# Kernel tuning notes

Measured on AMD Instinct MI355X. Metric: run time of the kernel, lower is better.

The kernel has to match this reference:

```python
import jax, jax.numpy as jnp
import numpy as np

B, T, E, H = 2, 2048, 1024, 16
D = E // H  # head_dim = 64


def setup_inputs() -> dict:
    key = jax.random.key(0)
    ks = jax.random.split(key, 7)
    s = 1.0 / np.sqrt(E)
    queries = jax.random.normal(ks[0], (B, T, E), dtype=jnp.float32)
    keys = jax.random.normal(ks[1], (B, T, E), dtype=jnp.float32)
    values = jax.random.normal(ks[2], (B, T, E), dtype=jnp.float32)
    # causal mask: True where attention is disallowed (masked_fill semantics)
    mask = jnp.triu(jnp.ones((T, T), dtype=bool), k=1)[None, None]  # [1,1,T,T]
    Wq = jax.random.uniform(ks[3], (E, E), jnp.float32, -s, s)
    Wk = jax.random.uniform(ks[4], (E, E), jnp.float32, -s, s)
    Wv = jax.random.uniform(ks[5], (E, E), jnp.float32, -s, s)
    Wo = jax.random.uniform(ks[6], (E, E), jnp.float32, -s, s)
    return {"queries": queries, "keys": keys, "values": values, "mask": mask,
            "Wq": Wq, "Wk": Wk, "Wv": Wv, "Wo": Wo}


def _split(x):
    # [B,T,E] -> [B,H,T,D]
    return x.reshape(B, T, H, D).transpose(0, 2, 1, 3)


def reference(queries, keys, values, mask, Wq, Wk, Wv, Wo):
    # nn.Linear(E,E,bias=False): y = x @ W.T
    q = _split(queries @ Wq.T)  # [B,H,T,D]
    k = _split(keys @ Wk.T)
    v = _split(values @ Wv.T)
    scores = jnp.einsum('bhqd,bhkd->bhqk', q, k) / jnp.sqrt(jnp.float32(D))
    scores = jnp.where(mask, -jnp.inf, scores)
    weights = jax.nn.softmax(scores, axis=-1)
    attn = jnp.einsum('bhqk,bhkd->bhqd', weights, v)  # [B,H,T,D]
    joined = attn.transpose(0, 2, 1, 3).reshape(B, T, E)
    return joined @ Wo.T
```

## Files before the change

kernel.cpp:

```cpp
#include <hip/hip_runtime.h>
#include <hip/hip_bf16.h>

#define T_DIM 2048
#define E_DIM 1024
#define MM 4096
#define NN 1024
#define KK 1024
#define MSZ ((size_t)MM * KK)
#define WSZ ((size_t)NN * KK)

typedef __attribute__((ext_vector_type(8))) short bh8;
typedef __attribute__((ext_vector_type(4))) short bh4;
typedef __attribute__((ext_vector_type(4))) float fx4;

static __device__ __forceinline__ short f2bf(float f) {
  union { float f; unsigned u; } v; v.f = f;
  unsigned r = (v.u + 0x7fffu + ((v.u >> 16) & 1u)) >> 16;
  return (short)(unsigned short)r;
}

static __device__ __forceinline__ void gload16(const void* g, void* l) {
  __builtin_amdgcn_global_load_lds(
      (const __attribute__((address_space(1))) unsigned*)g,
      (__attribute__((address_space(3))) unsigned*)l, 16, 0, 0);
}

__global__ __launch_bounds__(256) void cvt_w(const float* __restrict__ s0,
                                             const float* __restrict__ s1,
                                             const float* __restrict__ s2,
                                             const float* __restrict__ s3,
                                             short* __restrict__ dst) {
  int a = blockIdx.y;
  const float* sp = a == 0 ? s0 : a == 1 ? s1 : a == 2 ? s2 : s3;
  size_t i = ((size_t)blockIdx.x * 256 + threadIdx.x) * 8;
  fx4 x = *(const fx4*)(sp + i);
  fx4 y = *(const fx4*)(sp + i + 4);
  bh8 o;
#pragma unroll
  for (int j = 0; j < 4; j++) { o[j] = f2bf(x[j]); o[4 + j] = f2bf(y[j]); }
  *(bh8*)(dst + (size_t)a * WSZ + i) = o;
}

__global__ __launch_bounds__(256) void cvt_act(const float* __restrict__ s0,
                                               const float* __restrict__ s1,
                                               const float* __restrict__ s2,
                                               short* __restrict__ dst) {
  int a = blockIdx.y;
  const float* sp = a == 0 ? s0 : a == 1 ? s1 : s2;
  size_t i = ((size_t)blockIdx.x * 256 + threadIdx.x) * 8;
  fx4 x = *(const fx4*)(sp + i);
  fx4 y = *(const fx4*)(sp + i + 4);
  bh8 o;
#pragma unroll
  for (int j = 0; j < 4; j++) { o[j] = f2bf(x[j]); o[4 + j] = f2bf(y[j]); }
  *(bh8*)(dst + (size_t)a * MSZ + i) = o;
}

template<bool AF32, bool OUTF32>
__global__ __launch_bounds__(256) void gemm_fast(const void* __restrict__ A0,
                                                 const void* __restrict__ A1,
                                                 const void* __restrict__ A2,
                                                 const short* __restrict__ W0,
                                                 void* __restrict__ C0)
{
  __shared__ short As[128 * 32];
  __shared__ short Bs[128 * 32];
  const int tid = threadIdx.x;
  const int lane = tid & 63, w = tid >> 6;
  const int lm = lane & 15, lg = lane >> 4;
  const int wr = w >> 1, wc = w & 1;
  const int m0 = blockIdx.y * 128, n0 = blockIdx.x * 128;
  const int z = blockIdx.z;
  const void* Ap = z == 0 ? A0 : z == 1 ? A1 : A2;
  const short* W = W0 + (size_t)z * WSZ;

  fx4 acc[4][4] = {};

  for (int k0 = 0; k0 < KK; k0 += 32) {
    __syncthreads();
#pragma unroll
    for (int c = 0; c < 2; c++) {
      int idx = c * 256 + tid;
      int row = idx >> 2, kc = idx & 3;
      gload16(W + (size_t)(n0 + row) * KK + k0 + kc * 8, Bs + idx * 8);
      if constexpr (AF32) {
        const float* Af = (const float*)Ap;
        const float* src = Af + (size_t)(m0 + row) * KK + k0 + kc * 8;
        fx4 x = *(const fx4*)src;
        fx4 y = *(const fx4*)(src + 4);
        bh8 o;
#pragma unroll
        for (int j = 0; j < 4; j++) { o[j] = f2bf(x[j]); o[4 + j] = f2bf(y[j]); }
        *(bh8*)&As[idx * 8] = o;
      } else {
        const short* Ab = (const short*)Ap;
        gload16(Ab + (size_t)(m0 + row) * KK + k0 + kc * 8, As + idx * 8);
      }
    }
    __syncthreads();
    bh8 af[4], bf[4];
#pragma unroll
    for (int mi = 0; mi < 4; mi++)
      af[mi] = *(const bh8*)&As[(wr * 64 + mi * 16 + lm) * 32 + lg * 8];
#pragma unroll
    for (int ni = 0; ni < 4; ni++)
      bf[ni] = *(const bh8*)&Bs[(wc * 64 + ni * 16 + lm) * 32 + lg * 8];
#pragma unroll
    for (int mi = 0; mi < 4; mi++)
#pragma unroll
      for (int ni = 0; ni < 4; ni++)
        acc[mi][ni] = __builtin_amdgcn_mfma_f32_16x16x32_bf16(af[mi], bf[ni], acc[mi][ni], 0, 0, 0);
  }

#pragma unroll
  for (int mi = 0; mi < 4; mi++)
#pragma unroll
    for (int ni = 0; ni < 4; ni++) {
      int row = m0 + wr * 64 + mi * 16 + lg * 4;
      int col = n0 + wc * 64 + ni * 16 + lm;
#pragma unroll
      for (int r = 0; r < 4; r++) {
        float vv = acc[mi][ni][r];
        if constexpr (OUTF32) ((float*)C0)[(size_t)z * MSZ + (size_t)(row + r) * NN + col] = vv;
        else ((short*)C0)[(size_t)z * MSZ + (size_t)(row + r) * NN + col] = f2bf(vv);
      }
    }
}

template<bool AF32, bool OUTF32>
__global__ __launch_bounds__(256) void gemm_nt(const void* __restrict__ Ap,
                                               const float* __restrict__ Bw,
                                               void* __restrict__ Cp,
                                               int M, int N, int K)
{
  __shared__ short As[128 * 40];
  __shared__ short Bs[128 * 40];
  const int tid = threadIdx.x;
  const int lane = tid & 63;
  const int w = tid >> 6;
  const int lm = lane & 15;
  const int lg = lane >> 4;
  const int wr = w >> 1, wc = w & 1;
  const int m0 = blockIdx.y * 128, n0 = blockIdx.x * 128;

  fx4 acc[4][4] = {};

  for (int k0 = 0; k0 < K; k0 += 32) {
    __syncthreads();
#pragma unroll
    for (int i = 0; i < 4; ++i) {
      int g = i * 256 + tid;
      int row = g >> 3, cg = g & 7;
      bh4 a4;
      if constexpr (AF32) {
        const float* A = (const float*)Ap;
        fx4 v = *(const fx4*)(A + (size_t)(m0 + row) * K + k0 + cg * 4);
#pragma unroll
        for (int j = 0; j < 4; j++) a4[j] = f2bf(v[j]);
      } else {
        const short* A = (const short*)Ap;
        a4 = *(const bh4*)(A + (size_t)(m0 + row) * K + k0 + cg * 4);
      }
      *(bh4*)&As[row * 40 + cg * 4] = a4;

      fx4 bv = *(const fx4*)(Bw + (size_t)(n0 + row) * K + k0 + cg * 4);
      bh4 b4;
#pragma unroll
      for (int j = 0; j < 4; j++) b4[j] = f2bf(bv[j]);
      *(bh4*)&Bs[row * 40 + cg * 4] = b4;
    }
    __syncthreads();

    bh8 af[4], bf[4];
#pragma unroll
    for (int mi = 0; mi < 4; mi++)
      af[mi] = *(const bh8*)&As[(wr * 64 + mi * 16 + lm) * 40 + lg * 8];
#pragma unroll
    for (int ni = 0; ni < 4; ni++)
      bf[ni] = *(const bh8*)&Bs[(wc * 64 + ni * 16 + lm) * 40 + lg * 8];
#pragma unroll
    for (int mi = 0; mi < 4; mi++)
#pragma unroll
      for (int ni = 0; ni < 4; ni++)
        acc[mi][ni] = __builtin_amdgcn_mfma_f32_16x16x32_bf16(af[mi], bf[ni], acc[mi][ni], 0, 0, 0);
  }

#pragma unroll
  for (int mi = 0; mi < 4; mi++) {
#pragma unroll
    for (int ni = 0; ni < 4; ni++) {
      int row = m0 + wr * 64 + mi * 16 + lg * 4;
      int col = n0 + wc * 64 + ni * 16 + lm;
#pragma unroll
      for (int r = 0; r < 4; r++) {
        float vv = acc[mi][ni][r];
        if constexpr (OUTF32) ((float*)Cp)[(size_t)(row + r) * N + col] = vv;
        else        ((short*)Cp)[(size_t)(row + r) * N + col] = f2bf(vv);
      }
    }
  }
}

__global__ __launch_bounds__(256) void attn_kernel(const short* __restrict__ Q,
                                                   const short* __restrict__ Kb,
                                                   const short* __restrict__ Vb,
                                                   short* __restrict__ At)
{
  __shared__ short Kl[2][64 * 64];
  __shared__ short Vt[2][64 * 64];
  __shared__ short Pl[4 * 16 * 72];

  const int tid = threadIdx.x;
  const int lane = tid & 63;
  const int w = tid >> 6;
  const int lm = lane & 15;
  const int lg = lane >> 4;
  const int pi = blockIdx.x;
  const int bh = blockIdx.y;
  const size_t headoff = (size_t)(bh >> 4) * T_DIM * E_DIM + (size_t)(bh & 15) * 64;

  const int r0 = tid >> 3, ch0 = tid & 7;
  const int r1 = (256 + tid) >> 3, ch1 = tid & 7;

  for (int s = 0; s < 2; s++) {
    const int qt = s ? (31 - pi) : pi;
    const int q0 = qt * 64;

    const int qrow = q0 + w * 16 + lm;
    bh8 qf[2];
#pragma unroll
    for (int ks = 0; ks < 2; ks++)
      qf[ks] = *(const bh8*)(Q + headoff + (size_t)qrow * E_DIM + ks * 32 + lg * 8);

    fx4 oacc[4] = {};
    float m_r[4], l_r[4];
#pragma unroll
    for (int r = 0; r < 4; r++) { m_r[r] = -INFINITY; l_r[r] = 0.0f; }

    {
      gload16(Kb + headoff + (size_t)r0 * E_DIM + ((ch0 ^ (r0 & 7)) * 8), &Kl[0][tid * 8]);
      gload16(Kb + headoff + (size_t)r1 * E_DIM + ((ch1 ^ (r1 & 7)) * 8), &Kl[0][(256 + tid) * 8]);
      bh8 v8a = *(const bh8*)(Vb + headoff + (size_t)r0 * E_DIM + ch0 * 8);
      bh8 v8b = *(const bh8*)(Vb + headoff + (size_t)r1 * E_DIM + ch1 * 8);
#pragma unroll
      for (int j = 0; j < 8; j++) {
        int d = ch0 * 8 + j;
        Vt[0][d * 64 + (((r0 >> 3) ^ ((ch0 + j) & 7)) * 8) + (r0 & 7)] = v8a[j];
        Vt[0][d * 64 + (((r1 >> 3) ^ ((ch1 + j) & 7)) * 8) + (r1 & 7)] = v8b[j];
      }
    }
    __syncthreads();

    int cur = 0;
    for (int t = 0; t <= qt; ++t) {
      const bool pre = (t < qt);
      bh8 v8a, v8b;
      if (pre) {
        const int kvn = (t + 1) * 64;
        gload16(Kb + headoff + (size_t)(kvn + r0) * E_DIM + ((ch0 ^ (r0 & 7)) * 8),
                &Kl[cur ^ 1][tid * 8]);
        gload16(Kb + headoff + (size_t)(kvn + r1) * E_DIM + ((ch1 ^ (r1 & 7)) * 8),
                &Kl[cur ^ 1][(256 + tid) * 8]);
        v8a = *(const bh8*)(Vb + headoff + (size_t)(kvn + r0) * E_DIM + ch0 * 8);
        v8b = *(const bh8*)(Vb + headoff + (size_t)(kvn + r1) * E_DIM + ch1 * 8);
      }

      fx4 sacc[4] = {};
#pragma unroll
      for (int nb = 0; nb < 4; nb++) {
        const int rK = nb * 16 + lm;
#pragma unroll
        for (int ks = 0; ks < 2; ks++) {
          bh8 kf = *(const bh8*)&Kl[cur][rK * 64 + (((ks * 4 + lg) ^ (lm & 7)) * 8)];
          sacc[nb] = __builtin_amdgcn_mfma_f32_16x16x32_bf16(qf[ks], kf, sacc[nb], 0, 0, 0);
        }
      }

      float sv[4][4];
      const bool maskt = (t == qt);
#pragma unroll
      for (int nb = 0; nb < 4; nb++)
#pragma unroll
        for (int r = 0; r < 4; r++) {
          float x = sacc[nb][r] * 0.125f;
          if (maskt && (nb * 16 + lm > w * 16 + lg * 4 + r)) x = -INFINITY;
          sv[nb][r] = x;
        }

      float p[4][4];
#pragma unroll
      for (int r = 0; r < 4; r++) {
        float rm = fmaxf(fmaxf(sv[0][r], sv[1][r]), fmaxf(sv[2][r], sv[3][r]));
#pragma unroll
        for (int off = 1; off < 16; off <<= 1) rm = fmaxf(rm, __shfl_xor(rm, off));
        float mn = fmaxf(m_r[r], rm);
        float fac = __expf(m_r[r] - mn);
        float ps = 0.0f;
#pragma unroll
        for (int nb = 0; nb < 4; nb++) { p[nb][r] = __expf(sv[nb][r] - mn); ps += p[nb][r]; }
#pragma unroll
        for (int off = 1; off < 16; off <<= 1) ps += __shfl_xor(ps, off);
        l_r[r] = l_r[r] * fac + ps;
        m_r[r] = mn;
#pragma unroll
        for (int db = 0; db < 4; db++) oacc[db][r] *= fac;
      }

#pragma unroll
      for (int nb = 0; nb < 4; nb++)
#pragma unroll
        for (int r = 0; r < 4; r++)
          Pl[w * 1152 + (lg * 4 + r) * 72 + nb * 16 + lm] = f2bf(p[nb][r]);

      bh8 pa[2];
#pragma unroll
      for (int ks = 0; ks < 2; ks++)
        pa[ks] = *(const bh8*)&Pl[w * 1152 + lm * 72 + ks * 32 + lg * 8];
#pragma unroll
      for (int db = 0; db < 4; db++) {
        const int d = db * 16 + lm;
        const int gsw = ((d >> 3) + (d & 7)) & 7;
#pragma unroll
        for (int ks = 0; ks < 2; ks++) {
          bh8 vf = *(const bh8*)&Vt[cur][d * 64 + (((ks * 4 + lg) ^ gsw) * 8)];
          oacc[db] = __builtin_amdgcn_mfma_f32_16x16x32_bf16(pa[ks], vf, oacc[db], 0, 0, 0);
        }
      }

      if (pre) {
#pragma unroll
        for (int j = 0; j < 8; j++) {
          int d = ch0 * 8 + j;
          Vt[cur ^ 1][d * 64 + (((r0 >> 3) ^ ((ch0 + j) & 7)) * 8) + (r0 & 7)] = v8a[j];
          Vt[cur ^ 1][d * 64 + (((r1 >> 3) ^ ((ch1 + j) & 7)) * 8) + (r1 & 7)] = v8b[j];
        }
      }
      __syncthreads();
      cur ^= 1;
    }

#pragma unroll
    for (int r = 0; r < 4; r++) {
      float rl = 1.0f / l_r[r];
      int row = q0 + w * 16 + lg * 4 + r;
#pragma unroll
      for (int db = 0; db < 4; db++)
        At[headoff + (size_t)row * E_DIM + db * 16 + lm] = f2bf(oacc[db][r] * rl);
    }
  }
}

extern "C" void kernel_launch(void* const* d_in, const int* in_sizes, int n_in,
                              void* d_out, int out_size, void* d_ws, size_t ws_size,
                              hipStream_t stream)
{
  const float* q  = (const float*)d_in[0];
  const float* k  = (const float*)d_in[1];
  const float* v  = (const float*)d_in[2];
  const float* Wq = (const float*)d_in[4];
  const float* Wk = (const float*)d_in[5];
  const float* Wv = (const float*)d_in[6];
  const float* Wo = (const float*)d_in[7];

  short* Qb  = (short*)d_ws;
  short* Kbb = Qb + MSZ;
  short* Vbb = Kbb + MSZ;
  short* wqb = Vbb + MSZ;
  short* Xq  = wqb + 4 * WSZ;
  short* At  = Xq;

  const size_t need_full = (3 * MSZ + 4 * WSZ + 3 * MSZ) * 2;
  const size_t need_mid  = (4 * MSZ + 4 * WSZ) * 2;

  if (ws_size >= need_full) {
    cvt_act<<<dim3(MSZ / (256 * 8), 3), 256, 0, stream>>>(q, k, v, Xq);
    cvt_w<<<dim3(WSZ / (256 * 8), 4), 256, 0, stream>>>(Wq, Wk, Wv, Wo, wqb);
    gemm_fast<false, false><<<dim3(NN / 128, MM / 128, 3), 256, 0, stream>>>(
        Xq, Xq + MSZ, Xq + 2 * MSZ, wqb, Qb);
    attn_kernel<<<dim3(16, 32), 256, 0, stream>>>(Qb, Kbb, Vbb, At);
    gemm_fast<false, true><<<dim3(NN / 128, MM / 128, 1), 256, 0, stream>>>(
        At, At, At, wqb + 3 * WSZ, d_out);
  } else if (ws_size >= need_mid) {
    short* At2  = Vbb + MSZ;
    short* wqb2 = At2 + MSZ;
    cvt_w<<<dim3(WSZ / (256 * 8), 4), 256, 0, stream>>>(Wq, Wk, Wv, Wo, wqb2);
    gemm_fast<true, false><<<dim3(NN / 128, MM / 128, 3), 256, 0, stream>>>(q, k, v, wqb2, Qb);
    attn_kernel<<<dim3(16, 32), 256, 0, stream>>>(Qb, Kbb, Vbb, At2);
    gemm_fast<false, true><<<dim3(NN / 128, MM / 128, 1), 256, 0, stream>>>(
        At2, At2, At2, wqb2 + 3 * WSZ, d_out);
  } else {
    short* At2 = Vbb + MSZ;
    dim3 gg(NN / 128, MM / 128);
    gemm_nt<true, false><<<gg, 256, 0, stream>>>(q, Wq, Qb, MM, NN, KK);
    gemm_nt<true, false><<<gg, 256, 0, stream>>>(k, Wk, Kbb, MM, NN, KK);
    gemm_nt<true, false><<<gg, 256, 0, stream>>>(v, Wv, Vbb, MM, NN, KK);
    attn_kernel<<<dim3(16, 32), 256, 0, stream>>>(Qb, Kbb, Vbb, At2);
    gemm_nt<false, true><<<gg, 256, 0, stream>>>(At2, Wo, d_out, MM, NN, KK);
  }
}
```

Baseline: 262.8 us.

## Use DPP row reductions, exp2 softmax, XCD block swizzle and 64-row output GEMM

Replaces the shuffle-based 16-lane max and sum reductions in the attention softmax with DPP row_shr operations, and folds log2(e) into the score scale so exp2f can be used instead of __expf. Remaps attention and output-GEMM block indices with an XCD-aware swizzle so neighbouring tiles land on the same chiplet. Adds a dedicated output-projection GEMM with 64x128 tiles, doubling the block count to fill more CUs. The new GEMM has no double buffering or LDS swizzle, so it may lose per-block efficiency, and the DPP row_shr pattern relies on the row semantics of update_dpp being right for a full-row reduction.

```diff
diff --git a/kernel.cpp b/kernel.cpp
--- a/kernel.cpp
+++ b/kernel.cpp
@@ -23,6 +23,28 @@
   __builtin_amdgcn_global_load_lds(
       (const __attribute__((address_space(1))) unsigned*)g,
       (__attribute__((address_space(3))) unsigned*)l, 16, 0, 0);
+}
+
+template<int CTRL>
+static __device__ __forceinline__ float dppf(float x) {
+  union { float f; int i; } a, b;
+  a.f = x;
+  b.i = __builtin_amdgcn_update_dpp(0, a.i, CTRL, 0xf, 0xf, false);
+  return b.f;
+}
+static __device__ __forceinline__ float rowmax16(float x) {
+  x = fmaxf(x, dppf<0x121>(x));
+  x = fmaxf(x, dppf<0x122>(x));
+  x = fmaxf(x, dppf<0x124>(x));
+  x = fmaxf(x, dppf<0x128>(x));
+  return x;
+}
+static __device__ __forceinline__ float rowsum16(float x) {
+  x += dppf<0x121>(x);
+  x += dppf<0x122>(x);
+  x += dppf<0x124>(x);
+  x += dppf<0x128>(x);
+  return x;
 }
 
 __global__ __launch_bounds__(256) void cvt_w(const float* __restrict__ s0,
@@ -127,6 +149,60 @@
     }
 }
 
+__global__ __launch_bounds__(256) void gemm_out64(const short* __restrict__ A,
+                                                  const short* __restrict__ W,
+                                                  float* __restrict__ C)
+{
+  __shared__ short As[64 * 32];
+  __shared__ short Bs[128 * 32];
+  const int tid = threadIdx.x;
+  const int lane = tid & 63, w = tid >> 6;
+  const int lm = lane & 15, lg = lane >> 4;
+  const int lin = blockIdx.x + 8 * blockIdx.y;
+  const int swz = (lin & 7) * 64 + (lin >> 3);
+  const int n0 = (swz & 7) * 128, m0 = (swz >> 3) * 64;
+
+  fx4 acc[4][2] = {};
+
+  for (int k0 = 0; k0 < KK; k0 += 32) {
+    __syncthreads();
+    {
+      int row = tid >> 2, kc = tid & 3;
+      gload16(A + (size_t)(m0 + row) * KK + k0 + kc * 8, As + tid * 8);
+#pragma unroll
+      for (int c = 0; c < 2; c++) {
+        int idx = c * 256 + tid;
+        int brow = idx >> 2, bkc = idx & 3;
+        gload16(W + (size_t)(n0 + brow) * KK + k0 + bkc * 8, Bs + idx * 8);
+      }
+    }
+    __syncthreads();
+    bh8 af[4], bf[2];
+#pragma unroll
+    for (int mi = 0; mi < 4; mi++)
+      af[mi] = *(const bh8*)&As[(mi * 16 + lm) * 32 + lg * 8];
+#pragma unroll
+    for (int ni = 0; ni < 2; ni++)
+      bf[ni] = *(const bh8*)&Bs[(w * 32 + ni * 16 + lm) * 32 + lg * 8];
+#pragma unroll
+    for (int mi = 0; mi < 4; mi++)
+#pragma unroll
+      for (int ni = 0; ni < 2; ni++)
+        acc[mi][ni] = __builtin_amdgcn_mfma_f32_16x16x32_bf16(af[mi], bf[ni], acc[mi][ni], 0, 0, 0);
+  }
+
+#pragma unroll
+  for (int mi = 0; mi < 4; mi++)
+#pragma unroll
+    for (int ni = 0; ni < 2; ni++) {
+      int row = m0 + mi * 16 + lg * 4;
+      int col = n0 + w * 32 + ni * 16 + lm;
+#pragma unroll
+      for (int r = 0; r < 4; r++)
+        C[(size_t)(row + r) * NN + col] = acc[mi][ni][r];
+    }
+}
+
 template<bool AF32, bool OUTF32>
 __global__ __launch_bounds__(256) void gemm_nt(const void* __restrict__ Ap,
                                                const float* __restrict__ Bw,
@@ -215,9 +291,13 @@
   const int w = tid >> 6;
   const int lm = lane & 15;
   const int lg = lane >> 4;
-  const int pi = blockIdx.x;
-  const int bh = blockIdx.y;
+  const int lin = blockIdx.x + 16 * blockIdx.y;
+  const int swz = (lin & 7) * 64 + (lin >> 3);
+  const int pi = swz & 15;
+  const int bh = swz >> 4;
   const size_t headoff = (size_t)(bh >> 4) * T_DIM * E_DIM + (size_t)(bh & 15) * 64;
+
+  const float SCALE2 = 0.125f * 1.44269504f;
 
   const int r0 = tid >> 3, ch0 = tid & 7;
   const int r1 = (256 + tid) >> 3, ch1 = tid & 7;
@@ -282,7 +362,7 @@
       for (int nb = 0; nb < 4; nb++)
 #pragma unroll
         for (int r = 0; r < 4; r++) {
-          float x = sacc[nb][r] * 0.125f;
+          float x = sacc[nb][r] * SCALE2;
           if (maskt && (nb * 16 + lm > w * 16 + lg * 4 + r)) x = -INFINITY;
           sv[nb][r] = x;
         }
@@ -291,15 +371,13 @@
 #pragma unroll
       for (int r = 0; r < 4; r++) {
         float rm = fmaxf(fmaxf(sv[0][r], sv[1][r]), fmaxf(sv[2][r], sv[3][r]));
-#pragma unroll
-        for (int off = 1; off < 16; off <<= 1) rm = fmaxf(rm, __shfl_xor(rm, off));
+        rm = rowmax16(rm);
         float mn = fmaxf(m_r[r], rm);
-        float fac = __expf(m_r[r] - mn);
+        float fac = exp2f(m_r[r] - mn);
         float ps = 0.0f;
 #pragma unroll
-        for (int nb = 0; nb < 4; nb++) { p[nb][r] = __expf(sv[nb][r] - mn); ps += p[nb][r]; }
-#pragma unroll
-        for (int off = 1; off < 16; off <<= 1) ps += __shfl_xor(ps, off);
+        for (int nb = 0; nb < 4; nb++) { p[nb][r] = exp2f(sv[nb][r] - mn); ps += p[nb][r]; }
+        ps = rowsum16(ps);
         l_r[r] = l_r[r] * fac + ps;
         m_r[r] = mn;
 #pragma unroll
@@ -378,16 +456,16 @@
     gemm_fast<false, false><<<dim3(NN / 128, MM / 128, 3), 256, 0, stream>>>(
         Xq, Xq + MSZ, Xq + 2 * MSZ, wqb, Qb);
     attn_kernel<<<dim3(16, 32), 256, 0, stream>>>(Qb, Kbb, Vbb, At);
-    gemm_fast<false, true><<<dim3(NN / 128, MM / 128, 1), 256, 0, stream>>>(
-        At, At, At, wqb + 3 * WSZ, d_out);
+    gemm_out64<<<dim3(NN / 128, MM / 64), 256, 0, stream>>>(
+        At, wqb + 3 * WSZ, (float*)d_out);
   } else if (ws_size >= need_mid) {
     short* At2  = Vbb + MSZ;
     short* wqb2 = At2 + MSZ;
     cvt_w<<<dim3(WSZ / (256 * 8), 4), 256, 0, stream>>>(Wq, Wk, Wv, Wo, wqb2);
     gemm_fast<true, false><<<dim3(NN / 128, MM / 128, 3), 256, 0, stream>>>(q, k, v, wqb2, Qb);
     attn_kernel<<<dim3(16, 32), 256, 0, stream>>>(Qb, Kbb, Vbb, At2);
-    gemm_fast<false, true><<<dim3(NN / 128, MM / 128, 1), 256, 0, stream>>>(
-        At2, At2, At2, wqb2 + 3 * WSZ, d_out);
+    gemm_out64<<<dim3(NN / 128, MM / 64), 256, 0, stream>>>(
+        At2, wqb2 + 3 * WSZ, (float*)d_out);
   } else {
     short* At2 = Vbb + MSZ;
     dim3 gg(NN / 128, MM / 128);
```

After: 251.5 us. 1.04x faster.
